# Kernel optimization log

Measured on AMD Instinct MI355X. Metric: run time of the kernel, lower is better.

Reference implementation:

```python
import jax, jax.numpy as jnp
import numpy as np

KERNEL_MUL = 2.0
KERNEL_NUM = 5

def setup_inputs() -> dict:
    key = jax.random.key(0)
    k1, k2 = jax.random.split(key)
    source = jax.random.normal(k1, (4096, 256), dtype=jnp.float32)
    target = jax.random.normal(k2, (4096, 256), dtype=jnp.float32)
    return {"source": source, "target": target}

def reference(source, target):
    B = source.shape[0]
    total = jnp.concatenate([source, target], axis=0)           # [2N, D]
    n = total.shape[0]
    # pairwise squared L2 distances via expansion (same math as
    # ((total0 - total1)**2).sum(2) without the [2N,2N,D] intermediate)
    sq = jnp.sum(total * total, axis=-1)                         # [2N]
    l2 = jnp.maximum(sq[:, None] + sq[None, :] - 2.0 * (total @ total.T), 0.0)  # [2N,2N]
    # bandwidth from data mean of off-diagonal distances (detached in torch via .data)
    bandwidth = jax.lax.stop_gradient(jnp.sum(l2)) / (n * n - n)
    bandwidth = bandwidth / (KERNEL_MUL ** (KERNEL_NUM // 2))
    kernels = jnp.zeros_like(l2)
    for i in range(KERNEL_NUM):
        kernels = kernels + jnp.exp(-l2 / (bandwidth * (KERNEL_MUL ** i)))
    xx = kernels[:B, :B]
    yy = kernels[B:, B:]
    xy = kernels[:B, B:]
    yx = kernels[B:, :B]
    return jnp.mean(xx + yy - xy - yx)
```

## Files before the change

kernel.cpp:

```cpp
#include <hip/hip_runtime.h>


#define NROWS 8192
#define BHALF 4096
#define DDIM  256
#define TILE  128
#define NTILE 64
#define NBLK  2080

typedef __attribute__((ext_vector_type(8))) short bf16x8;
typedef __attribute__((ext_vector_type(4))) float f32x4;
typedef __attribute__((ext_vector_type(2))) float f32x2;
typedef __attribute__((ext_vector_type(4))) unsigned short u16x4;

struct Ws {
  float coef;
  float Spart[256];
  float cpart[256][256];
  float sq[NROWS];
  float part[NBLK];
};

__device__ __forceinline__ unsigned short f2bf(float x) {
  unsigned int u = __builtin_bit_cast(unsigned int, x);
  return (unsigned short)((u + 0x7fffu + ((u >> 16) & 1u)) >> 16);
}

__device__ __forceinline__ const float* row_ptr(const float* src, const float* tgt, int i) {
  return (i < BHALF) ? (src + (size_t)i * DDIM) : (tgt + (size_t)(i - BHALF) * DDIM);
}

__global__ __launch_bounds__(256) void k_prep(const float* __restrict__ src,
                                              const float* __restrict__ tgt,
                                              Ws* __restrict__ ws,
                                              unsigned short* __restrict__ tb,
                                              int conv) {
  __shared__ float cls[4][256];
  __shared__ float sred[4];
  int tid = threadIdx.x, wave = tid >> 6, lane = tid & 63;
  int row0 = blockIdx.x * 32 + wave * 8;
  float c0 = 0.f, c1 = 0.f, c2 = 0.f, c3 = 0.f;
  float s[8];
  #pragma unroll
  for (int r = 0; r < 8; ++r) {
    const float4* rp = (const float4*)row_ptr(src, tgt, row0 + r);
    float4 x = rp[lane];
    if (conv) {
      u16x4 b = { f2bf(x.x), f2bf(x.y), f2bf(x.z), f2bf(x.w) };
      *(u16x4*)&tb[(size_t)(row0 + r) * DDIM + lane * 4] = b;
    }
    c0 += x.x; c1 += x.y; c2 += x.z; c3 += x.w;
    s[r] = x.x * x.x + x.y * x.y + x.z * x.z + x.w * x.w;
  }
  #pragma unroll
  for (int off = 32; off > 0; off >>= 1) {
    #pragma unroll
    for (int r = 0; r < 8; ++r) s[r] += __shfl_xor(s[r], off);
  }
  if (lane == 0) {
    float Sw = 0.f;
    #pragma unroll
    for (int r = 0; r < 8; ++r) { ws->sq[row0 + r] = s[r]; Sw += s[r]; }
    sred[wave] = Sw;
  }
  cls[wave][lane * 4 + 0] = c0;
  cls[wave][lane * 4 + 1] = c1;
  cls[wave][lane * 4 + 2] = c2;
  cls[wave][lane * 4 + 3] = c3;
  __syncthreads();
  ws->cpart[blockIdx.x][tid] = cls[0][tid] + cls[1][tid] + cls[2][tid] + cls[3][tid];
  if (tid == 0) ws->Spart[blockIdx.x] = sred[0] + sred[1] + sred[2] + sred[3];
}

__global__ __launch_bounds__(256) void k_bw(Ws* __restrict__ ws) {
  __shared__ float redm[4], reds[4];
  int tid = threadIdx.x, wave = tid >> 6, lane = tid & 63;
  float mc = 0.f;
  for (int b0 = 0; b0 < 256; b0 += 16) {
    float v[16];
    #pragma unroll
    for (int j = 0; j < 16; ++j) v[j] = ws->cpart[b0 + j][tid];
    #pragma unroll
    for (int j = 0; j < 16; ++j) mc += v[j];
  }
  float p = mc * mc;
  float sp = ws->Spart[tid];
  #pragma unroll
  for (int off = 32; off > 0; off >>= 1) {
    p  += __shfl_xor(p, off);
    sp += __shfl_xor(sp, off);
  }
  if (lane == 0) { redm[wave] = p; reds[wave] = sp; }
  __syncthreads();
  if (tid == 0) {
    float msq = redm[0] + redm[1] + redm[2] + redm[3];
    float S   = reds[0] + reds[1] + reds[2] + reds[3];
    double n = (double)NROWS;
    double sum_l2 = 2.0 * n * (double)S - 2.0 * (double)msq;
    double bw = sum_l2 / (n * n - n) / 4.0;
    ws->coef = (float)(1.4426950408889634 / (16.0 * bw));
  }
}

__device__ __forceinline__ void stage_tiles(const unsigned short* gA,
                                            const unsigned short* gB,
                                            unsigned short* lA, unsigned short* lB,
                                            int kc) {
  #pragma unroll
  for (int t = 0; t < 4; ++t) {
    __builtin_amdgcn_global_load_lds(
        (const __attribute__((address_space(1))) void*)(gA + (size_t)(t * 8) * DDIM + kc * 64),
        (__attribute__((address_space(3))) void*)(lA + (t * 8) * 64), 16, 0, 0);
    __builtin_amdgcn_global_load_lds(
        (const __attribute__((address_space(1))) void*)(gB + (size_t)(t * 8) * DDIM + kc * 64),
        (__attribute__((address_space(3))) void*)(lB + (t * 8) * 64), 16, 0, 0);
  }
}

template <int FAST>
__global__ __launch_bounds__(256, 4) void k_main(const unsigned short* __restrict__ tb,
                                                 const float* __restrict__ src,
                                                 const float* __restrict__ tgt,
                                                 Ws* __restrict__ ws) {
  int bid = blockIdx.x;
  int idx = (bid & 7) * (NBLK / 8) + (bid >> 3);
  int ti = (int)((129.0 - sqrt(129.0 * 129.0 - 8.0 * (double)idx)) * 0.5);
  while (64 * (ti + 1) - ((ti + 1) * ti) / 2 <= idx) ++ti;
  while (64 * ti - (ti * (ti - 1)) / 2 > idx) --ti;
  int tj = ti + (idx - (64 * ti - (ti * (ti - 1)) / 2));

  __shared__ __align__(16) unsigned short As[TILE * 64];
  __shared__ __align__(16) unsigned short Bs[TILE * 64];
  __shared__ float wsum[4];

  int tid = threadIdx.x;
  int wave = tid >> 6, lane = tid & 63;
  int wm = wave >> 1, wn = wave & 1;
  int lr = lane & 15, q = lane >> 4;
  int Ib = ti * TILE, Jb = tj * TILE;

  f32x4 zero = {0.f, 0.f, 0.f, 0.f};
  f32x4 acc[4][4];
  #pragma unroll
  for (int m = 0; m < 4; ++m)
    #pragma unroll
    for (int n = 0; n < 4; ++n) acc[m][n] = zero;

  const unsigned short* gA = nullptr; const unsigned short* gB = nullptr;
  if (FAST) {
    int lrow = lane >> 3;
    int lchk = (lane & 7) ^ lrow;
    gA = tb + (size_t)(Ib + wave * 32 + lrow) * DDIM + lchk * 8;
    gB = tb + (size_t)(Jb + wave * 32 + lrow) * DDIM + lchk * 8;
  }
  int r0 = tid >> 4, c4 = tid & 15;

  #pragma unroll
  for (int kc = 0; kc < 4; ++kc) {
    if (kc) __syncthreads();
    if (FAST) {
      stage_tiles(gA, gB, &As[(wave * 32) * 64], &Bs[(wave * 32) * 64], kc);
    } else {
      #pragma unroll
      for (int rr = 0; rr < 8; ++rr) {
        int row = rr * 16 + r0;
        int sw = ((c4 >> 1) ^ (row & 7)) * 8 + (c4 & 1) * 4;
        float4 va = ((const float4*)row_ptr(src, tgt, Ib + row))[kc * 16 + c4];
        u16x4 ba = { f2bf(va.x), f2bf(va.y), f2bf(va.z), f2bf(va.w) };
        *(u16x4*)&As[row * 64 + sw] = ba;
        float4 vb = ((const float4*)row_ptr(src, tgt, Jb + row))[kc * 16 + c4];
        u16x4 bb = { f2bf(vb.x), f2bf(vb.y), f2bf(vb.z), f2bf(vb.w) };
        *(u16x4*)&Bs[row * 64 + sw] = bb;
      }
    }
    __syncthreads();
    #pragma unroll
    for (int kk = 0; kk < 2; ++kk) {
      int cidx = ((kk * 4 + q) ^ (lr & 7)) << 3;
      bf16x8 af[4], bfr[4];
      #pragma unroll
      for (int m = 0; m < 4; ++m)
        af[m] = *(const bf16x8*)&As[(wm * 64 + m * 16 + lr) * 64 + cidx];
      #pragma unroll
      for (int n = 0; n < 4; ++n)
        bfr[n] = *(const bf16x8*)&Bs[(wn * 64 + n * 16 + lr) * 64 + cidx];
      #pragma unroll
      for (int m = 0; m < 4; ++m)
        #pragma unroll
        for (int n = 0; n < 4; ++n)
          acc[m][n] = __builtin_amdgcn_mfma_f32_16x16x32_bf16(af[m], bfr[n], acc[m][n], 0, 0, 0);
    }
  }

  float coef = ws->coef;
  float coef2 = 2.f * coef;
  int ibase = Ib + wm * 64;
  int jbase = Jb + wn * 64;
  float nscj[4];
  f32x2 nsci01[4], nsci23[4];
  #pragma unroll
  for (int n = 0; n < 4; ++n) nscj[n] = -ws->sq[jbase + n * 16 + lr] * coef;
  #pragma unroll
  for (int m = 0; m < 4; ++m) {
    nsci01[m] = f32x2{ -ws->sq[ibase + m * 16 + q * 4 + 0] * coef,
                       -ws->sq[ibase + m * 16 + q * 4 + 1] * coef };
    nsci23[m] = f32x2{ -ws->sq[ibase + m * 16 + q * 4 + 2] * coef,
                       -ws->sq[ibase + m * 16 + q * 4 + 3] * coef };
  }

  const f32x2 c2v = { coef2, coef2 };
  f32x2 accA = {0.f, 0.f}, accB = {0.f, 0.f};
  f32x2 accC = {0.f, 0.f}, accD = {0.f, 0.f};
  #pragma unroll
  for (int m = 0; m < 4; ++m) {
    #pragma unroll
    for (int n = 0; n < 4; ++n) {
      f32x4 g = acc[m][n];
      f32x2 bj = { nscj[n], nscj[n] };
      f32x2 b01 = nsci01[m] + bj;
      f32x2 b23 = nsci23[m] + bj;
      f32x2 a01 = f32x2{g[0], g[1]} * c2v + b01;
      f32x2 a23 = f32x2{g[2], g[3]} * c2v + b23;
      f32x2 t0, t1;
      t0.x = __builtin_amdgcn_exp2f(a01.x); t0.y = __builtin_amdgcn_exp2f(a01.y);
      t1.x = __builtin_amdgcn_exp2f(a23.x); t1.y = __builtin_amdgcn_exp2f(a23.y);
      f32x2 p0 = t0 * t0, p1 = t1 * t1;
      f32x2 q0 = p0 * p0, q1 = p1 * p1;
      f32x2 r0v = q0 * q0, r1v = q1 * q1;
      accA += t0 + p0;
      accB += q0 + r0v;
      accA = r0v * r0v + accA;
      accC += t1 + p1;
      accD += q1 + r1v;
      accC = r1v * r1v + accC;
    }
  }
  float lsum = (accA.x + accA.y) + (accB.x + accB.y)
             + (accC.x + accC.y) + (accD.x + accD.y);
  #pragma unroll
  for (int off = 32; off > 0; off >>= 1) lsum += __shfl_xor(lsum, off);
  if (lane == 0) wsum[wave] = lsum;
  __syncthreads();
  if (tid == 0) {
    float tot = wsum[0] + wsum[1] + wsum[2] + wsum[3];
    float sA = (ti < 32) ? 1.f : -1.f;
    float sB = (tj < 32) ? 1.f : -1.f;
    float fac = sA * sB * ((ti == tj) ? 1.f : 2.f);
    ws->part[blockIdx.x] = fac * tot;
  }
}

__global__ __launch_bounds__(256) void k_final(const Ws* __restrict__ ws,
                                               float* __restrict__ out) {
  __shared__ double red[4];
  int tid = threadIdx.x, wave = tid >> 6, lane = tid & 63;
  double s = 0.0;
  for (int i = tid; i < NBLK; i += 256) s += (double)ws->part[i];
  #pragma unroll
  for (int off = 32; off > 0; off >>= 1) s += __shfl_xor(s, off);
  if (lane == 0) red[wave] = s;
  __syncthreads();
  if (tid == 0)
    out[0] = (float)((red[0] + red[1] + red[2] + red[3]) /
                     ((double)BHALF * (double)BHALF));
}

extern "C" void kernel_launch(void* const* d_in, const int* in_sizes, int n_in,
                              void* d_out, int out_size, void* d_ws, size_t ws_size,
                              hipStream_t stream) {
  const float* src = (const float*)d_in[0];
  const float* tgt = (const float*)d_in[1];
  Ws* ws = (Ws*)d_ws;
  float* out = (float*)d_out;

  size_t wsoff = (sizeof(Ws) + 255) & ~(size_t)255;
  size_t need = wsoff + (size_t)NROWS * DDIM * 2;
  bool fast = ws_size >= need;
  unsigned short* tb = fast ? (unsigned short*)((char*)d_ws + wsoff) : nullptr;

  hipLaunchKernelGGL(k_prep, dim3(256), dim3(256), 0, stream, src, tgt, ws, tb,
                     fast ? 1 : 0);
  hipLaunchKernelGGL(k_bw, dim3(1), dim3(256), 0, stream, ws);
  if (fast)
    hipLaunchKernelGGL((k_main<1>), dim3(NBLK), dim3(256), 0, stream, tb, src, tgt, ws);
  else
    hipLaunchKernelGGL((k_main<0>), dim3(NBLK), dim3(256), 0, stream, tb, src, tgt, ws);
  hipLaunchKernelGGL(k_final, dim3(1), dim3(256), 0, stream, ws, out);
}
```

Measured before the change: 99.23 us.

## Double-buffer K-slices in main GEMM and fuse final reduction via last-block atomic

Splits the 256-deep K loop into eight 32-wide slices and stages the next slice into a second LDS buffer while MFMAs run on the current one, with a new XOR swizzle for the narrower rows. This hides global-to-LDS latency and halves the LDS footprint per buffer, at the cost of more barriers per tile. It also removes the separate k_final launch: each block atomically increments a counter and the last block reduces all partials and writes the output, saving one kernel launch but adding an atomic per block.

```diff
diff --git a/kernel.cpp b/kernel.cpp
--- a/kernel.cpp
+++ b/kernel.cpp
@@ -5,6 +5,7 @@
 #define BHALF 4096
 #define DDIM  256
 #define TILE  128
+#define BK    32
 #define NTILE 64
 #define NBLK  2080
 
@@ -15,6 +16,7 @@
 
 struct Ws {
   float coef;
+  unsigned int cnt;
   float Spart[256];
   float cpart[256][256];
   float sq[NROWS];
@@ -75,6 +77,7 @@
 __global__ __launch_bounds__(256) void k_bw(Ws* __restrict__ ws) {
   __shared__ float redm[4], reds[4];
   int tid = threadIdx.x, wave = tid >> 6, lane = tid & 63;
+  if (tid == 0) ws->cnt = 0u;
   float mc = 0.f;
   for (int b0 = 0; b0 < 256; b0 += 16) {
     float v[16];
@@ -102,18 +105,18 @@
   }
 }
 
-__device__ __forceinline__ void stage_tiles(const unsigned short* gA,
-                                            const unsigned short* gB,
-                                            unsigned short* lA, unsigned short* lB,
-                                            int kc) {
-  #pragma unroll
-  for (int t = 0; t < 4; ++t) {
+__device__ __forceinline__ void stage32(const unsigned short* gA,
+                                        const unsigned short* gB,
+                                        unsigned short* lA, unsigned short* lB,
+                                        int kcs) {
+  #pragma unroll
+  for (int t = 0; t < 2; ++t) {
     __builtin_amdgcn_global_load_lds(
-        (const __attribute__((address_space(1))) void*)(gA + (size_t)(t * 8) * DDIM + kc * 64),
-        (__attribute__((address_space(3))) void*)(lA + (t * 8) * 64), 16, 0, 0);
+        (const __attribute__((address_space(1))) void*)(gA + (size_t)(t * 16) * DDIM + kcs * BK),
+        (__attribute__((address_space(3))) void*)(lA + (t * 16) * BK), 16, 0, 0);
     __builtin_amdgcn_global_load_lds(
-        (const __attribute__((address_space(1))) void*)(gB + (size_t)(t * 8) * DDIM + kc * 64),
-        (__attribute__((address_space(3))) void*)(lB + (t * 8) * 64), 16, 0, 0);
+        (const __attribute__((address_space(1))) void*)(gB + (size_t)(t * 16) * DDIM + kcs * BK),
+        (__attribute__((address_space(3))) void*)(lB + (t * 16) * BK), 16, 0, 0);
   }
 }
 
@@ -121,7 +124,8 @@
 __global__ __launch_bounds__(256, 4) void k_main(const unsigned short* __restrict__ tb,
                                                  const float* __restrict__ src,
                                                  const float* __restrict__ tgt,
-                                                 Ws* __restrict__ ws) {
+                                                 Ws* __restrict__ ws,
+                                                 float* __restrict__ out) {
   int bid = blockIdx.x;
   int idx = (bid & 7) * (NBLK / 8) + (bid >> 3);
   int ti = (int)((129.0 - sqrt(129.0 * 129.0 - 8.0 * (double)idx)) * 0.5);
@@ -129,9 +133,11 @@
   while (64 * ti - (ti * (ti - 1)) / 2 > idx) --ti;
   int tj = ti + (idx - (64 * ti - (ti * (ti - 1)) / 2));
 
-  __shared__ __align__(16) unsigned short As[TILE * 64];
-  __shared__ __align__(16) unsigned short Bs[TILE * 64];
+  __shared__ __align__(16) unsigned short As[2][TILE * BK];
+  __shared__ __align__(16) unsigned short Bs[2][TILE * BK];
   __shared__ float wsum[4];
+  __shared__ double dred[4];
+  __shared__ unsigned int slast;
 
   int tid = threadIdx.x;
   int wave = tid >> 6, lane = tid & 63;
@@ -146,44 +152,76 @@
     #pragma unroll
     for (int n = 0; n < 4; ++n) acc[m][n] = zero;
 
-  const unsigned short* gA = nullptr; const unsigned short* gB = nullptr;
+  const int coff = ((q ^ ((lr >> 1) & 3)) << 3);
+
   if (FAST) {
-    int lrow = lane >> 3;
-    int lchk = (lane & 7) ^ lrow;
-    gA = tb + (size_t)(Ib + wave * 32 + lrow) * DDIM + lchk * 8;
-    gB = tb + (size_t)(Jb + wave * 32 + lrow) * DDIM + lchk * 8;
-  }
-  int r0 = tid >> 4, c4 = tid & 15;
-
-  #pragma unroll
-  for (int kc = 0; kc < 4; ++kc) {
-    if (kc) __syncthreads();
-    if (FAST) {
-      stage_tiles(gA, gB, &As[(wave * 32) * 64], &Bs[(wave * 32) * 64], kc);
-    } else {
-      #pragma unroll
-      for (int rr = 0; rr < 8; ++rr) {
-        int row = rr * 16 + r0;
-        int sw = ((c4 >> 1) ^ (row & 7)) * 8 + (c4 & 1) * 4;
-        float4 va = ((const float4*)row_ptr(src, tgt, Ib + row))[kc * 16 + c4];
-        u16x4 ba = { f2bf(va.x), f2bf(va.y), f2bf(va.z), f2bf(va.w) };
-        *(u16x4*)&As[row * 64 + sw] = ba;
-        float4 vb = ((const float4*)row_ptr(src, tgt, Jb + row))[kc * 16 + c4];
-        u16x4 bb = { f2bf(vb.x), f2bf(vb.y), f2bf(vb.z), f2bf(vb.w) };
-        *(u16x4*)&Bs[row * 64 + sw] = bb;
+    int lrow = lane >> 2;
+    int lchk = (lane & 3) ^ ((lane >> 3) & 3);
+    const unsigned short* gA = tb + (size_t)(Ib + wave * 32 + lrow) * DDIM + lchk * 8;
+    const unsigned short* gB = tb + (size_t)(Jb + wave * 32 + lrow) * DDIM + lchk * 8;
+    unsigned short* lA0 = &As[0][wave * 32 * BK];
+    unsigned short* lB0 = &Bs[0][wave * 32 * BK];
+    unsigned short* lA1 = &As[1][wave * 32 * BK];
+    unsigned short* lB1 = &Bs[1][wave * 32 * BK];
+
+    stage32(gA, gB, lA0, lB0, 0);
+    __syncthreads();
+    #pragma unroll
+    for (int kcs = 0; kcs < 8; ++kcs) {
+      if (kcs < 7)
+        stage32(gA, gB, ((kcs + 1) & 1) ? lA1 : lA0,
+                        ((kcs + 1) & 1) ? lB1 : lB0, kcs + 1);
+      const unsigned short* Ab = As[kcs & 1];
+      const unsigned short* Bb = Bs[kcs & 1];
+      bf16x8 af[4], bfr[4];
+      #pragma unroll
+      for (int m = 0; m < 4; ++m)
+        af[m] = *(const bf16x8*)&Ab[(wm * 64 + m * 16 + lr) * BK + coff];
+      #pragma unroll
+      for (int n = 0; n < 4; ++n)
+        bfr[n] = *(const bf16x8*)&Bb[(wn * 64 + n * 16 + lr) * BK + coff];
+      #pragma unroll
+      for (int m = 0; m < 4; ++m)
+        #pragma unroll
+        for (int n = 0; n < 4; ++n)
+          acc[m][n] = __builtin_amdgcn_mfma_f32_16x16x32_bf16(af[m], bfr[n], acc[m][n], 0, 0, 0);
+      if (kcs < 7) __syncthreads();
+    }
+  } else {
+    int row = tid >> 1, h = tid & 1;
+    int fsw = (row >> 1) & 3;
+    const float4* rpA = (const float4*)row_ptr(src, tgt, Ib + row);
+    const float4* rpB = (const float4*)row_ptr(src, tgt, Jb + row);
+    #pragma unroll
+    for (int kcs = 0; kcs < 8; ++kcs) {
+      if (kcs) __syncthreads();
+      unsigned short* lA = As[kcs & 1];
+      unsigned short* lB = Bs[kcs & 1];
+      #pragma unroll
+      for (int cc = 0; cc < 2; ++cc) {
+        int c = h * 2 + cc;
+        int slot = c ^ fsw;
+        float4 v0 = rpA[kcs * 8 + c * 2], v1 = rpA[kcs * 8 + c * 2 + 1];
+        u16x4 a0 = { f2bf(v0.x), f2bf(v0.y), f2bf(v0.z), f2bf(v0.w) };
+        u16x4 a1 = { f2bf(v1.x), f2bf(v1.y), f2bf(v1.z), f2bf(v1.w) };
+        *(u16x4*)&lA[row * BK + slot * 8]     = a0;
+        *(u16x4*)&lA[row * BK + slot * 8 + 4] = a1;
+        float4 w0 = rpB[kcs * 8 + c * 2], w1 = rpB[kcs * 8 + c * 2 + 1];
+        u16x4 b0 = { f2bf(w0.x), f2bf(w0.y), f2bf(w0.z), f2bf(w0.w) };
+        u16x4 b1 = { f2bf(w1.x), f2bf(w1.y), f2bf(w1.z), f2bf(w1.w) };
+        *(u16x4*)&lB[row * BK + slot * 8]     = b0;
+        *(u16x4*)&lB[row * BK + slot * 8 + 4] = b1;
       }
-    }
-    __syncthreads();
-    #pragma unroll
-    for (int kk = 0; kk < 2; ++kk) {
-      int cidx = ((kk * 4 + q) ^ (lr & 7)) << 3;
+      __syncthreads();
+      const unsigned short* Ab = As[kcs & 1];
+      const unsigned short* Bb = Bs[kcs & 1];
       bf16x8 af[4], bfr[4];
       #pragma unroll
       for (int m = 0; m < 4; ++m)
-        af[m] = *(const bf16x8*)&As[(wm * 64 + m * 16 + lr) * 64 + cidx];
+        af[m] = *(const bf16x8*)&Ab[(wm * 64 + m * 16 + lr) * BK + coff];
       #pragma unroll
       for (int n = 0; n < 4; ++n)
-        bfr[n] = *(const bf16x8*)&Bs[(wn * 64 + n * 16 + lr) * 64 + cidx];
+        bfr[n] = *(const bf16x8*)&Bb[(wn * 64 + n * 16 + lr) * BK + coff];
       #pragma unroll
       for (int m = 0; m < 4; ++m)
         #pragma unroll
@@ -241,28 +279,32 @@
   for (int off = 32; off > 0; off >>= 1) lsum += __shfl_xor(lsum, off);
   if (lane == 0) wsum[wave] = lsum;
   __syncthreads();
+
   if (tid == 0) {
     float tot = wsum[0] + wsum[1] + wsum[2] + wsum[3];
     float sA = (ti < 32) ? 1.f : -1.f;
     float sB = (tj < 32) ? 1.f : -1.f;
     float fac = sA * sB * ((ti == tj) ? 1.f : 2.f);
-    ws->part[blockIdx.x] = fac * tot;
-  }
-}
-
-__global__ __launch_bounds__(256) void k_final(const Ws* __restrict__ ws,
-                                               float* __restrict__ out) {
-  __shared__ double red[4];
-  int tid = threadIdx.x, wave = tid >> 6, lane = tid & 63;
-  double s = 0.0;
-  for (int i = tid; i < NBLK; i += 256) s += (double)ws->part[i];
-  #pragma unroll
-  for (int off = 32; off > 0; off >>= 1) s += __shfl_xor(s, off);
-  if (lane == 0) red[wave] = s;
+    __hip_atomic_store(&ws->part[blockIdx.x], fac * tot,
+                       __ATOMIC_RELAXED, __HIP_MEMORY_SCOPE_AGENT);
+    unsigned int old = __hip_atomic_fetch_add(&ws->cnt, 1u,
+                       __ATOMIC_ACQ_REL, __HIP_MEMORY_SCOPE_AGENT);
+    slast = (old == NBLK - 1) ? 1u : 0u;
+  }
   __syncthreads();
-  if (tid == 0)
-    out[0] = (float)((red[0] + red[1] + red[2] + red[3]) /
-                     ((double)BHALF * (double)BHALF));
+  if (slast) {
+    double s = 0.0;
+    for (int i = tid; i < NBLK; i += 256)
+      s += (double)__hip_atomic_load(&ws->part[i],
+                     __ATOMIC_RELAXED, __HIP_MEMORY_SCOPE_AGENT);
+    #pragma unroll
+    for (int off = 32; off > 0; off >>= 1) s += __shfl_xor(s, off);
+    if (lane == 0) dred[wave] = s;
+    __syncthreads();
+    if (tid == 0)
+      out[0] = (float)((dred[0] + dred[1] + dred[2] + dred[3]) /
+                       ((double)BHALF * (double)BHALF));
+  }
 }
 
 extern "C" void kernel_launch(void* const* d_in, const int* in_sizes, int n_in,
@@ -282,8 +324,7 @@
                      fast ? 1 : 0);
   hipLaunchKernelGGL(k_bw, dim3(1), dim3(256), 0, stream, ws);
   if (fast)
-    hipLaunchKernelGGL((k_main<1>), dim3(NBLK), dim3(256), 0, stream, tb, src, tgt, ws);
+    hipLaunchKernelGGL((k_main<1>), dim3(NBLK), dim3(256), 0, stream, tb, src, tgt, ws, out);
   else
-    hipLaunchKernelGGL((k_main<0>), dim3(NBLK), dim3(256), 0, stream, tb, src, tgt, ws);
-  hipLaunchKernelGGL(k_final, dim3(1), dim3(256), 0, stream, ws, out);
-}
+    hipLaunchKernelGGL((k_main<0>), dim3(NBLK), dim3(256), 0, stream, tb, src, tgt, ws, out);
+}
```

Result: slower. 127.7 us (+28.7%).
